# Kernel tuning notes

Measured on AMD Instinct MI355X. Metric: run time of the kernel, lower is better.

## Reference

```python
import jax, jax.numpy as jnp
import numpy as np

K = 0.5  # bottom-k fraction from __init__


def setup_inputs() -> dict:
    key = jax.random.key(0)
    k1, k2 = jax.random.split(key)
    N, V = 8192, 32000
    outputs = jax.random.normal(k1, (N, V), dtype=jnp.float32)
    labels = jax.random.randint(k2, (N,), 0, V, dtype=jnp.int64)
    return {"outputs": outputs, "labels": labels}


def reference(outputs, labels):
    # per-sample cross entropy: logsumexp(logits) - logits[label]
    N = outputs.shape[0]
    logZ = jax.nn.logsumexp(outputs, axis=-1)                             # [N]
    picked = jnp.take_along_axis(outputs, labels[:, None], axis=-1)[:, 0]  # [N]
    ce = logZ - picked                                                     # [N]
    m = int(N * K)  # number of smallest losses kept (K in (0,1])
    # bottom-k via top_k on negated losses (avoids full sort)
    neg_bottom, _ = jax.lax.top_k(-ce, m)
    return jnp.mean(-neg_bottom)
```

## Files before the change

### kernel.cpp

```cpp
#include <hip/hip_runtime.h>
#include <math.h>


#define MAX_N 8192

__global__ __launch_bounds__(256) void ce_rows(const float* __restrict__ logits,
                                               const int* __restrict__ labels,
                                               float* __restrict__ ce, int V) {
    const int row = blockIdx.x;
    const float* rp = logits + (size_t)row * V;
    const float4* rp4 = (const float4*)rp;
    const int V4 = V >> 2;

    float s0 = 0.f, s1 = 0.f, s2 = 0.f, s3 = 0.f;
    for (int j = threadIdx.x; j < V4; j += 256) {
        float4 v = rp4[j];
        s0 += __expf(v.x);
        s1 += __expf(v.y);
        s2 += __expf(v.z);
        s3 += __expf(v.w);
    }
    for (int j = (V4 << 2) + threadIdx.x; j < V; j += 256) s0 += __expf(rp[j]);

    float s = (s0 + s1) + (s2 + s3);
    #pragma unroll
    for (int off = 32; off > 0; off >>= 1) s += __shfl_down(s, off, 64);

    __shared__ float wsum[4];
    const int lane = threadIdx.x & 63, wid = threadIdx.x >> 6;
    if (lane == 0) wsum[wid] = s;
    __syncthreads();
    if (threadIdx.x == 0) {
        float tot = (wsum[0] + wsum[1]) + (wsum[2] + wsum[3]);
        float picked = rp[labels[row]];
        ce[row] = logf(tot) - picked;
    }
}

__device__ __forceinline__ unsigned f2k(float f) {
    unsigned u = __float_as_uint(f);
    return (u & 0x80000000u) ? ~u : (u | 0x80000000u);
}
__device__ __forceinline__ float k2f(unsigned k) {
    unsigned u = (k & 0x80000000u) ? (k ^ 0x80000000u) : ~k;
    return __uint_as_float(u);
}

__global__ __launch_bounds__(1024) void bottomk_mean(const float* __restrict__ ce,
                                                     float* __restrict__ out,
                                                     int n, int m) {
    __shared__ unsigned keys[MAX_N];
    __shared__ unsigned hist[256];
    __shared__ unsigned s_prefix, s_remaining;
    const int tid = threadIdx.x;

    for (int i = tid; i < n; i += 1024) keys[i] = f2k(ce[i]);
    if (tid == 0) { s_prefix = 0u; s_remaining = (unsigned)m; }
    __syncthreads();

    unsigned prefmask = 0u;
    for (int shift = 24; shift >= 0; shift -= 8) {
        if (tid < 256) hist[tid] = 0u;
        __syncthreads();
        const unsigned prefix = s_prefix;
        for (int i = tid; i < n; i += 1024) {
            unsigned k = keys[i];
            if ((k & prefmask) == prefix) atomicAdd(&hist[(k >> shift) & 255u], 1u);
        }
        __syncthreads();
        if (tid == 0) {
            unsigned rem = s_remaining, cum = 0u;
            int b = 0;
            for (; b < 256; ++b) {
                if (cum + hist[b] >= rem) break;
                cum += hist[b];
            }
            s_prefix = prefix | ((unsigned)b << shift);
            s_remaining = rem - cum;
        }
        prefmask |= (255u << shift);
        __syncthreads();
    }

    const unsigned T = s_prefix;
    float lsum = 0.f;
    unsigned lcnt = 0u;
    for (int i = tid; i < n; i += 1024) {
        unsigned k = keys[i];
        if (k < T) { lsum += k2f(k); lcnt++; }
    }
    #pragma unroll
    for (int off = 32; off > 0; off >>= 1) {
        lsum += __shfl_down(lsum, off, 64);
        lcnt += __shfl_down(lcnt, off, 64);
    }
    __shared__ float wsum[16];
    __shared__ unsigned wcnt[16];
    const int lane = tid & 63, wid = tid >> 6;
    if (lane == 0) { wsum[wid] = lsum; wcnt[wid] = lcnt; }
    __syncthreads();
    if (tid == 0) {
        float tot = 0.f;
        unsigned cnt = 0u;
        const int nw = (1024 + 63) / 64;
        for (int w = 0; w < nw; ++w) { tot += wsum[w]; cnt += wcnt[w]; }
        tot += (float)((unsigned)m - cnt) * k2f(T);
        out[0] = tot / (float)m;
    }
}

extern "C" void kernel_launch(void* const* d_in, const int* in_sizes, int n_in,
                              void* d_out, int out_size, void* d_ws, size_t ws_size,
                              hipStream_t stream) {
    const float* logits = (const float*)d_in[0];
    const int* labels = (const int*)d_in[1];
    float* out = (float*)d_out;
    float* ce = (float*)d_ws;

    const int N = in_sizes[1];
    const int V = in_sizes[0] / N;
    const int M = N / 2;

    ce_rows<<<N, 256, 0, stream>>>(logits, labels, ce, V);
    bottomk_mean<<<1, 1024, 0, stream>>>(ce, out, N, M);
}
```

Baseline: 224.7 us.

## Process one row per wavefront with nontemporal unrolled loads in CE kernel

Changes the per-row cross-entropy kernel so each 64-lane wavefront handles a whole row (four rows per block) rather than one row per 256-thread block. This removes the shared-memory reduction and block barrier. The loop is unrolled two-deep using nontemporal vector loads, and logf is replaced by the faster __logf. The trade-offs are fewer loads in flight per row and slightly reduced log precision.

```diff
diff --git a/kernel.cpp b/kernel.cpp
--- a/kernel.cpp
+++ b/kernel.cpp
@@ -4,36 +4,42 @@
 
 #define MAX_N 8192
 
+typedef float f32x4 __attribute__((ext_vector_type(4)));
+
 __global__ __launch_bounds__(256) void ce_rows(const float* __restrict__ logits,
                                                const int* __restrict__ labels,
-                                               float* __restrict__ ce, int V) {
-    const int row = blockIdx.x;
+                                               float* __restrict__ ce, int n, int V) {
+    const int lane = threadIdx.x & 63;
+    const int wid = threadIdx.x >> 6;
+    const int row = blockIdx.x * 4 + wid;
+    if (row >= n) return;
+
     const float* rp = logits + (size_t)row * V;
-    const float4* rp4 = (const float4*)rp;
+    const f32x4* rp4 = (const f32x4*)rp;
     const int V4 = V >> 2;
 
     float s0 = 0.f, s1 = 0.f, s2 = 0.f, s3 = 0.f;
-    for (int j = threadIdx.x; j < V4; j += 256) {
-        float4 v = rp4[j];
-        s0 += __expf(v.x);
-        s1 += __expf(v.y);
-        s2 += __expf(v.z);
-        s3 += __expf(v.w);
+    float s4 = 0.f, s5 = 0.f, s6 = 0.f, s7 = 0.f;
+    int j = lane;
+    for (; j + 64 < V4; j += 128) {
+        f32x4 a = __builtin_nontemporal_load(&rp4[j]);
+        f32x4 b = __builtin_nontemporal_load(&rp4[j + 64]);
+        s0 += __expf(a.x); s1 += __expf(a.y); s2 += __expf(a.z); s3 += __expf(a.w);
+        s4 += __expf(b.x); s5 += __expf(b.y); s6 += __expf(b.z); s7 += __expf(b.w);
     }
-    for (int j = (V4 << 2) + threadIdx.x; j < V; j += 256) s0 += __expf(rp[j]);
+    for (; j < V4; j += 64) {
+        f32x4 a = __builtin_nontemporal_load(&rp4[j]);
+        s0 += __expf(a.x); s1 += __expf(a.y); s2 += __expf(a.z); s3 += __expf(a.w);
+    }
+    for (int t = (V4 << 2) + lane; t < V; t += 64) s0 += __expf(rp[t]);
 
-    float s = (s0 + s1) + (s2 + s3);
+    float s = ((s0 + s1) + (s2 + s3)) + ((s4 + s5) + (s6 + s7));
     #pragma unroll
     for (int off = 32; off > 0; off >>= 1) s += __shfl_down(s, off, 64);
 
-    __shared__ float wsum[4];
-    const int lane = threadIdx.x & 63, wid = threadIdx.x >> 6;
-    if (lane == 0) wsum[wid] = s;
-    __syncthreads();
-    if (threadIdx.x == 0) {
-        float tot = (wsum[0] + wsum[1]) + (wsum[2] + wsum[3]);
+    if (lane == 0) {
         float picked = rp[labels[row]];
-        ce[row] = logf(tot) - picked;
+        ce[row] = __logf(s) - picked;
     }
 }
 
@@ -121,6 +127,7 @@
     const int V = in_sizes[0] / N;
     const int M = N / 2;
 
-    ce_rows<<<N, 256, 0, stream>>>(logits, labels, ce, V);
+    const int rows_per_block = 4;
+    ce_rows<<<(N + rows_per_block - 1) / rows_per_block, 256, 0, stream>>>(logits, labels, ce, N, V);
     bottomk_mean<<<1, 1024, 0, stream>>>(ce, out, N, M);
 }
```

Result: faster. 210.9 us (-6.2%).
